# Optimization experiments

Measured on AMD Instinct MI355X. Metric: run time of the kernel, lower is better.

Reference implementation:

```python
import jax, jax.numpy as jnp
import numpy as np

NUM_LAYERS = 4
HID = 512
EMB = 512
VOCAB = 50000
SOU_LEN = 256
TAR_LEN = 50
BATCH = 8
VEXT = VOCAB + SOU_LEN


def _gru_layer(x, h0, wih, whh, bih, bhh):
    # x: [B,T,in], h0: [B,H]; PyTorch GRU gate order: r, z, n
    def step(h, xt):
        gi = xt @ wih.T + bih
        gh = h @ whh.T + bhh
        ir, iz, inn = jnp.split(gi, 3, axis=-1)
        hr, hz, hn = jnp.split(gh, 3, axis=-1)
        r = jax.nn.sigmoid(ir + hr)
        z = jax.nn.sigmoid(iz + hz)
        n = jnp.tanh(inn + r * hn)
        h_new = (1.0 - z) * n + z * h
        return h_new, h_new
    _, ys = jax.lax.scan(step, h0, jnp.swapaxes(x, 0, 1))
    return jnp.swapaxes(ys, 0, 1)


def _forward(sou, tar, hidden, encoder_outputs, extended_length,
             emb, gru_wih, gru_whh, gru_bih, gru_bhh,
             fc_enc_w, fc_enc_b, fc_dec_w, fc_dec_b, v_w,
             fc_out1_w, fc_out1_b, fc_out2_w, fc_out2_b,
             g1_w, g1_b, g2_w, g2_b, g3_w, g3_b):
    emb = emb.at[0].set(0.0)  # padding_idx=0 (also zeroes its grad)
    tar_emb = emb[tar]  # [B,T,E]
    # pack_padded_sequence: only first `length` steps processed, rest padded with 0
    lengths = jnp.maximum(jnp.sum(tar > 0, axis=-1), 1)
    x = tar_emb
    for l in range(gru_wih.shape[0]):
        x = _gru_layer(x, hidden[l], gru_wih[l], gru_whh[l], gru_bih[l], gru_bhh[l])
    t_idx = jnp.arange(x.shape[1])
    dec_out = jnp.where((t_idx[None, :] < lengths[:, None])[:, :, None], x, 0.0)  # [B,T,H]
    # additive (Bahdanau) attention
    e1 = encoder_outputs @ fc_enc_w.T + fc_enc_b          # [B,S,H]
    e2 = dec_out @ fc_dec_w.T + fc_dec_b                  # [B,T,H]
    energy = jnp.tanh(e1[:, None, :, :] + e2[:, :, None, :])  # [B,T,S,H]
    scores = jnp.einsum('btsh,h->bts', energy, v_w)
    scores = jnp.where((sou == 0)[:, None, :], -jnp.inf, scores)
    atten = jax.nn.softmax(scores, axis=-1)               # [B,T,S]
    weighted = jnp.einsum('bts,bsh->bth', atten, encoder_outputs)
    all_out = jnp.concatenate([weighted, dec_out], axis=-1)  # [B,T,2H]
    mid = all_out @ fc_out2_w.T + fc_out2_b
    logits = mid @ fc_out1_w.T + fc_out1_b                # [B,T,VEXT]
    # extended-vocab mask (vectorized version of the per-batch python loop)
    col = jnp.arange(logits.shape[-1])
    valid = col[None, None, :] < (VOCAB + extended_length)[:, None, None]
    logits = jnp.where(valid, logits, -1e9)
    output_gen = jax.nn.softmax(logits, axis=-1)
    # copy mechanism: scatter-add attention into extended vocab (replaces sparse one-hot bmm)
    def _scatter(att_b, sou_b):
        return jnp.zeros((att_b.shape[0], VEXT), att_b.dtype).at[:, sou_b].add(att_b)
    output_copy = jax.vmap(_scatter)(atten, sou)          # [B,T,VEXT]
    gate = jax.nn.sigmoid(
        jnp.einsum('bth,h->bt', weighted, g1_w) + g1_b[0]
        + jnp.einsum('bth,h->bt', dec_out, g2_w) + g2_b[0]
        + jnp.einsum('bte,e->bt', tar_emb, g3_w) + g3_b[0])[:, :, None]
    output = (1.0 - gate) * output_gen + gate * output_copy
    return output, atten


def setup_inputs() -> dict:
    key = jax.random.key(0)
    ks = jax.random.split(key, 24)
    s = 0.02
    return {
        'sou': jax.random.randint(ks[0], (BATCH, SOU_LEN), 0, VEXT),
        'tar': jax.random.randint(ks[1], (BATCH, TAR_LEN), 0, VEXT),
        'hidden': jax.random.normal(ks[2], (NUM_LAYERS, BATCH, HID), jnp.float32),
        'encoder_outputs': jax.random.normal(ks[3], (BATCH, SOU_LEN, HID), jnp.float32),
        'extended_length': jax.random.randint(ks[4], (BATCH,), 0, SOU_LEN),
        'emb': jax.random.normal(ks[5], (VEXT, EMB), jnp.float32) * s,
        'gru_wih': jax.random.normal(ks[6], (NUM_LAYERS, 3 * HID, EMB), jnp.float32) * s,
        'gru_whh': jax.random.normal(ks[7], (NUM_LAYERS, 3 * HID, HID), jnp.float32) * s,
        'gru_bih': jax.random.normal(ks[8], (NUM_LAYERS, 3 * HID), jnp.float32) * s,
        'gru_bhh': jax.random.normal(ks[9], (NUM_LAYERS, 3 * HID), jnp.float32) * s,
        'fc_enc_w': jax.random.normal(ks[10], (HID, HID), jnp.float32) * s,
        'fc_enc_b': jax.random.normal(ks[11], (HID,), jnp.float32) * s,
        'fc_dec_w': jax.random.normal(ks[12], (HID, HID), jnp.float32) * s,
        'fc_dec_b': jax.random.normal(ks[13], (HID,), jnp.float32) * s,
        'v_w': jax.random.normal(ks[14], (HID,), jnp.float32) * s,
        'fc_out1_w': jax.random.normal(ks[15], (VEXT, HID), jnp.float32) * s,
        'fc_out1_b': jax.random.normal(ks[16], (VEXT,), jnp.float32) * s,
        'fc_out2_w': jax.random.normal(ks[17], (HID, 2 * HID), jnp.float32) * s,
        'fc_out2_b': jax.random.normal(ks[18], (HID,), jnp.float32) * s,
        'g1_w': jax.random.normal(ks[19], (HID,), jnp.float32) * s,
        'g1_b': jnp.zeros((1,), jnp.float32),
        'g2_w': jax.random.normal(ks[20], (HID,), jnp.float32) * s,
        'g2_b': jnp.zeros((1,), jnp.float32),
        'g3_w': jax.random.normal(ks[21], (EMB,), jnp.float32) * s,
        'g3_b': jnp.zeros((1,), jnp.float32),
    }


def reference(sou, tar, hidden, encoder_outputs, extended_length,
              emb, gru_wih, gru_whh, gru_bih, gru_bhh,
              fc_enc_w, fc_enc_b, fc_dec_w, fc_dec_b, v_w,
              fc_out1_w, fc_out1_b, fc_out2_w, fc_out2_b,
              g1_w, g1_b, g2_w, g2_b, g3_w, g3_b):
    return _forward(sou, tar, hidden, encoder_outputs, extended_length,
                    emb, gru_wih, gru_whh, gru_bih, gru_bhh,
                    fc_enc_w, fc_enc_b, fc_dec_w, fc_dec_b, v_w,
                    fc_out1_w, fc_out1_b, fc_out2_w, fc_out2_b,
                    g1_w, g1_b, g2_w, g2_b, g3_w, g3_b)
```

## Files before the change

### kernel.cpp

```cpp
#include <hip/hip_runtime.h>

typedef unsigned short u16;
typedef unsigned int u32;
typedef unsigned long long u64;

using bf16x8 = __attribute__((ext_vector_type(8))) short;
using f32x4  = __attribute__((ext_vector_type(4))) float;

#define VOCAB 50000
#define VEXT  50256
#define OUT_AT_OFF 20102400L

__device__ __forceinline__ u16 f2b(float f) {
  u32 x = __float_as_uint(f);
  u32 r = (x + 0x7fffu + ((x >> 16) & 1u)) >> 16;
  return (u16)r;
}

__device__ __forceinline__ u32 sload32(const u32* p) {
  return __hip_atomic_load(p, __ATOMIC_RELAXED, __HIP_MEMORY_SCOPE_SYSTEM);
}
__device__ __forceinline__ u64 sload64(const u64* p) {
  return __hip_atomic_load(p, __ATOMIC_RELAXED, __HIP_MEMORY_SCOPE_SYSTEM);
}
__device__ __forceinline__ void sstore64(u64* p, u64 v) {
  __hip_atomic_store(p, v, __ATOMIC_RELAXED, __HIP_MEMORY_SCOPE_SYSTEM);
}
__device__ __forceinline__ bf16x8 sload8x(const u64* p) {
  union { u64 u[2]; bf16x8 v; } x;
  x.u[0] = sload64(p); x.u[1] = sload64(p + 1);
  return x.v;
}
__device__ __forceinline__ void wait_cnt(const u32* c, u32 target) {
  unsigned it = 0;
  while (sload32(c) < target) {
    __builtin_amdgcn_s_sleep(2);
    if (++it > (1u << 20)) break;
  }
  asm volatile("" ::: "memory");
}

__global__ void k_conv(const float* __restrict__ src, u16* __restrict__ dst,
                       long realN, long totalN) {
  long i = (long)blockIdx.x * 256 + threadIdx.x;
  if (i >= totalN) return;
  float v = (i < realN) ? src[i] : 0.f;
  dst[i] = f2b(v);
}

__global__ void k_h0b(const float* __restrict__ hidden, u16* __restrict__ h0B) {
  int i = blockIdx.x * 256 + threadIdx.x;
  int l = i >> 13, rem = i & 8191, rr = rem >> 9, k = rem & 511;
  float v = (rr < 8) ? hidden[((long)l * 8 + rr) * 512 + k] : 0.f;
  h0B[i] = f2b(v);
}

__global__ __launch_bounds__(256) void k_prep(const int* __restrict__ tar,
                                              const float* __restrict__ emb,
                                              const float* __restrict__ g3w,
                                              u16* __restrict__ xB0,
                                              float* __restrict__ g3dot) {
  int r = blockIdx.x;
  int tid = threadIdx.x;
  int idx = tar[r];
  __shared__ float red[256];
  float p = 0.f;
  for (int k = tid; k < 512; k += 256) {
    float v = (idx == 0) ? 0.f : emb[(long)idx * 512 + k];
    xB0[(long)r * 512 + k] = f2b(v);
    p += v * g3w[k];
  }
  red[tid] = p; __syncthreads();
  for (int o = 128; o > 0; o >>= 1) { if (tid < o) red[tid] += red[tid + o]; __syncthreads(); }
  if (tid == 0) g3dot[r] = red[0];
}

__global__ void k_lengths(const int* __restrict__ tar, int* __restrict__ lens) {
  int b = threadIdx.x;
  if (b < 8) {
    int c = 0;
    for (int t = 0; t < 50; t++) c += (tar[b * 50 + t] > 0) ? 1 : 0;
    lens[b] = (c > 0) ? c : 1;
  }
}

__global__ __launch_bounds__(256) void k_mask(float* __restrict__ x4f,
                                              const int* __restrict__ lens) {
  int r = blockIdx.x, b = r / 50, t = r % 50;
  if (t >= lens[b])
    for (int k = threadIdx.x; k < 512; k += 256) x4f[(long)r * 512 + k] = 0.f;
}

__global__ __launch_bounds__(128, 1) void k_gru(
    const u16* __restrict__ wihB, const u16* __restrict__ whhB,
    const float* __restrict__ bih, const float* __restrict__ bhh,
    const float* __restrict__ hidden, const u16* __restrict__ h0B,
    u16* __restrict__ xB,
    u32* __restrict__ hX,
    float* __restrict__ x4f,
    u32* __restrict__ cnt)
{
  const int wg = blockIdx.x;
  const int l = wg >> 5;
  const int c0 = (wg & 31) << 4;
  const int tid = threadIdx.x;
  const int wv = tid >> 6;
  const int lane = tid & 63;
  const int lrow = lane & 15;
  const int q = lane >> 4;

  __shared__ float giX[2][3][16][16];

  const u16* Wsrc = (wv == 0 ? wihB : whhB) + (long)l * 1536 * 512;

  const int col = c0 + lrow;
  const float bir = bih[l * 1536 + col],         bhr = bhh[l * 1536 + col];
  const float biz = bih[l * 1536 + 512 + col],   bhz = bhh[l * 1536 + 512 + col];
  const float bin_ = bih[l * 1536 + 1024 + col], bhn = bhh[l * 1536 + 1024 + col];

  const u16* xin = xB + (long)l * 16 * 50 * 512;

  float hreg[4];
  if (wv == 1) {
#pragma unroll
    for (int rg = 0; rg < 4; rg++) {
      int bb = q * 4 + rg;
      hreg[rg] = (bb < 8) ? hidden[((long)l * 8 + bb) * 512 + col] : 0.f;
    }
  }

  for (int t = 0; t < 50; t++) {
    bf16x8 af[16];
    if (wv == 0) {
      if (l > 0) {
        wait_cnt(cnt + (l - 1) * 16, 32u * (u32)(t + 1));
        const u64* A64 = (const u64*)((const u32*)xin + (long)lrow * 50 * 256 + (long)t * 256);
#pragma unroll
        for (int ks = 0; ks < 16; ks++) af[ks] = sload8x(A64 + ks * 8 + q * 2);
      } else {
        const u16* Asrc = xin + (long)lrow * 50 * 512 + (long)t * 512;
#pragma unroll
        for (int ks = 0; ks < 16; ks++) af[ks] = *(const bf16x8*)(Asrc + ks * 32 + q * 8);
      }
    } else {
      if (t > 0) {
        wait_cnt(cnt + l * 16, 32u * (u32)t);
        const u64* H64 = (const u64*)(hX + (((long)l * 2 + ((t - 1) & 1)) * 16 + lrow) * 256);
#pragma unroll
        for (int ks = 0; ks < 16; ks++) af[ks] = sload8x(H64 + ks * 8 + q * 2);
      } else {
        const u16* Asrc = h0B + ((long)l * 16 + lrow) * 512;
#pragma unroll
        for (int ks = 0; ks < 16; ks++) af[ks] = *(const bf16x8*)(Asrc + ks * 32 + q * 8);
      }
    }

    f32x4 a0 = {0.f, 0.f, 0.f, 0.f}, a1 = {0.f, 0.f, 0.f, 0.f}, a2 = {0.f, 0.f, 0.f, 0.f};
#pragma unroll
    for (int ks = 0; ks < 16; ks++) {
      bf16x8 b0 = *(const bf16x8*)(Wsrc + (long)(0 * 512 + c0 + lrow) * 512 + ks * 32 + q * 8);
      bf16x8 b1 = *(const bf16x8*)(Wsrc + (long)(1 * 512 + c0 + lrow) * 512 + ks * 32 + q * 8);
      bf16x8 b2 = *(const bf16x8*)(Wsrc + (long)(2 * 512 + c0 + lrow) * 512 + ks * 32 + q * 8);
      a0 = __builtin_amdgcn_mfma_f32_16x16x32_bf16(af[ks], b0, a0, 0, 0, 0);
      a1 = __builtin_amdgcn_mfma_f32_16x16x32_bf16(af[ks], b1, a1, 0, 0, 0);
      a2 = __builtin_amdgcn_mfma_f32_16x16x32_bf16(af[ks], b2, a2, 0, 0, 0);
    }

    if (wv == 0) {
#pragma unroll
      for (int rg = 0; rg < 4; rg++) {
        giX[t & 1][0][q * 4 + rg][lrow] = a0[rg];
        giX[t & 1][1][q * 4 + rg][lrow] = a1[rg];
        giX[t & 1][2][q * 4 + rg][lrow] = a2[rg];
      }
    }
    __syncthreads();

    if (wv == 1) {
#pragma unroll
      for (int rg = 0; rg < 4; rg++) {
        int bb = q * 4 + rg;
        float hnew = 0.f;
        u16 hb16 = 0;
        if (bb < 8) {
          float gir = giX[t & 1][0][bb][lrow] + bir;
          float giz = giX[t & 1][1][bb][lrow] + biz;
          float gin = giX[t & 1][2][bb][lrow] + bin_;
          float ghr = a0[rg] + bhr;
          float ghz = a1[rg] + bhz;
          float ghn = a2[rg] + bhn;
          float hprev = hreg[rg];
          float rr = 1.f / (1.f + expf(-(gir + ghr)));
          float zz = 1.f / (1.f + expf(-(giz + ghz)));
          float nn = tanhf(gin + rr * ghn);
          hnew = (1.f - zz) * nn + zz * hprev;
          hreg[rg] = hnew;
          hb16 = f2b(hnew);
        }
        u32 p32 = (u32)hb16 | ((u32)(u16)__shfl_xor((int)hb16, 1) << 16);
        u64 p64 = (u64)p32 | ((u64)(u32)__shfl_xor((int)p32, 2) << 32);
        if (bb < 8) {
          if ((lrow & 3) == 0) {
            long slot = ((long)l * 2 + (t & 1)) * 16 + bb;
            sstore64((u64*)hX + slot * 128 + (col >> 2), p64);
            if (l < 3)
              sstore64((u64*)xB + ((((long)(l + 1) * 16 + bb) * 50 + t) * 128) + (col >> 2), p64);
          }
          if (l == 3) x4f[((long)bb * 50 + t) * 512 + col] = hnew;
        }
      }
      asm volatile("s_waitcnt vmcnt(0)" ::: "memory");
      if (lane == 0)
        __hip_atomic_fetch_add(cnt + (long)l * 16, 1u,
                               __ATOMIC_RELAXED, __HIP_MEMORY_SCOPE_SYSTEM);
    }
  }
}

__global__ __launch_bounds__(256, 2) void k_gemm_bf16(
    const u16* __restrict__ A, const u16* __restrict__ Bm,
    const float* __restrict__ bias, float* __restrict__ C,
    int M, int N, int K, int ldc)
{
  __shared__ __align__(16) u16 As[4096];
  __shared__ __align__(16) u16 Bs[4096];
  const int tid = threadIdx.x;
  const int wv = tid >> 6, lane = tid & 63;
  const int wm = wv >> 1, wn = wv & 1;
  const int lrow = lane & 15, q = lane >> 4;
  const int m0 = blockIdx.y * 128, n0 = blockIdx.x * 128;

  f32x4 acc[4][4];
#pragma unroll
  for (int i = 0; i < 4; i++)
#pragma unroll
    for (int j = 0; j < 4; j++) acc[i][j] = {0.f, 0.f, 0.f, 0.f};

  for (int k0 = 0; k0 < K; k0 += 32) {
#pragma unroll
    for (int i = 0; i < 2; i++) {
      int c = i * 256 + tid;
      int row = c >> 2, ko = (c & 3) << 3;
      *(uint4*)(As + c * 8) = *(const uint4*)(A + (long)(m0 + row) * K + k0 + ko);
      *(uint4*)(Bs + c * 8) = *(const uint4*)(Bm + (long)(n0 + row) * K + k0 + ko);
    }
    __syncthreads();
    bf16x8 af[4], bfr[4];
#pragma unroll
    for (int i = 0; i < 4; i++) af[i] = *(const bf16x8*)(As + (wm * 64 + i * 16 + lrow) * 32 + q * 8);
#pragma unroll
    for (int j = 0; j < 4; j++) bfr[j] = *(const bf16x8*)(Bs + (wn * 64 + j * 16 + lrow) * 32 + q * 8);
#pragma unroll
    for (int i = 0; i < 4; i++)
#pragma unroll
      for (int j = 0; j < 4; j++)
        acc[i][j] = __builtin_amdgcn_mfma_f32_16x16x32_bf16(af[i], bfr[j], acc[i][j], 0, 0, 0);
    __syncthreads();
  }

#pragma unroll
  for (int i = 0; i < 4; i++) {
    int rbase = m0 + wm * 64 + i * 16 + q * 4;
#pragma unroll
    for (int j = 0; j < 4; j++) {
      int colg = n0 + wn * 64 + j * 16 + lrow;
      if (colg < N) {
        float bv = bias[colg];
#pragma unroll
        for (int rg = 0; rg < 4; rg++) {
          int rowg = rbase + rg;
          if (rowg < M) C[(long)rowg * ldc + colg] = acc[i][j][rg] + bv;
        }
      }
    }
  }
}

__global__ __launch_bounds__(256) void k_attn(
    const float* __restrict__ e1, const float* __restrict__ e2,
    const float* __restrict__ enc, const float* __restrict__ x4f,
    const int* __restrict__ sou, const float* __restrict__ vw,
    const float* __restrict__ g1w, const float* __restrict__ g1b,
    const float* __restrict__ g2w, const float* __restrict__ g2b,
    const float* __restrict__ g3b, const float* __restrict__ g3dot,
    float* __restrict__ all_out, float* __restrict__ gate,
    float* __restrict__ atten_out)
{
  int r = blockIdx.x;
  int b = r / 50;
  int tid = threadIdx.x;
  __shared__ float e2s[512], decs[512], at[256], red[256];
  for (int k = tid; k < 512; k += 256) {
    e2s[k] = e2[(long)r * 512 + k];
    decs[k] = x4f[(long)r * 512 + k];
  }
  __syncthreads();
  const float* erow = e1 + ((long)b * 256 + tid) * 512;
  float sc = 0.f;
#pragma unroll 4
  for (int h = 0; h < 512; h++) sc += vw[h] * tanhf(erow[h] + e2s[h]);
  if (sou[b * 256 + tid] == 0) sc = -INFINITY;

  red[tid] = sc; __syncthreads();
  for (int o = 128; o > 0; o >>= 1) { if (tid < o) red[tid] = fmaxf(red[tid], red[tid + o]); __syncthreads(); }
  float mx = red[0]; __syncthreads();
  float p = expf(sc - mx);
  red[tid] = p; __syncthreads();
  for (int o = 128; o > 0; o >>= 1) { if (tid < o) red[tid] += red[tid + o]; __syncthreads(); }
  float S = red[0]; __syncthreads();
  float a = p / S;
  at[tid] = a;
  atten_out[(long)r * 256 + tid] = a;
  __syncthreads();

  float pg = 0.f;
  for (int h = tid; h < 512; h += 256) {
    float wsum = 0.f;
    const float* ecol = enc + (long)b * 256 * 512 + h;
    for (int s = 0; s < 256; s++) wsum += at[s] * ecol[(long)s * 512];
    all_out[(long)r * 1024 + h] = wsum;
    all_out[(long)r * 1024 + 512 + h] = decs[h];
    pg += wsum * g1w[h] + decs[h] * g2w[h];
  }
  red[tid] = pg; __syncthreads();
  for (int o = 128; o > 0; o >>= 1) { if (tid < o) red[tid] += red[tid + o]; __syncthreads(); }
  if (tid == 0) {
    float z = red[0] + g1b[0] + g2b[0] + g3dot[r] + g3b[0];
    gate[r] = 1.f / (1.f + expf(-z));
  }
}

__global__ __launch_bounds__(1024) void k_softmax(float* __restrict__ out,
                                                  const float* __restrict__ gate,
                                                  const int* __restrict__ ext) {
  int r = blockIdx.x;
  int b = r / 50;
  int tid = threadIdx.x;
  int nv = VOCAB + ext[b];
  __shared__ float red[1024];
  float* row = out + (long)r * VEXT;
  float m = -INFINITY;
  for (int c = tid; c < nv; c += 1024) m = fmaxf(m, row[c]);
  red[tid] = m; __syncthreads();
  for (int o = 512; o > 0; o >>= 1) { if (tid < o) red[tid] = fmaxf(red[tid], red[tid + o]); __syncthreads(); }
  m = red[0]; __syncthreads();
  float s = 0.f;
  for (int c = tid; c < nv; c += 1024) s += expf(row[c] - m);
  red[tid] = s; __syncthreads();
  for (int o = 512; o > 0; o >>= 1) { if (tid < o) red[tid] += red[tid + o]; __syncthreads(); }
  float inv = (1.f - gate[r]) / red[0];
  for (int c = tid; c < VEXT; c += 1024) {
    float v = (c < nv) ? expf(row[c] - m) * inv : 0.f;
    row[c] = v;
  }
}

__global__ void k_scatter(float* __restrict__ out, const float* __restrict__ atten,
                          const float* __restrict__ gate, const int* __restrict__ sou) {
  int r = blockIdx.x, s = threadIdx.x;
  int b = r / 50;
  float v = gate[r] * atten[(long)r * 256 + s];
  int colv = sou[b * 256 + s];
  atomicAdd(out + (long)r * VEXT + colv, v);
}

extern "C" void kernel_launch(void* const* d_in, const int* in_sizes, int n_in,
                              void* d_out, int out_size, void* d_ws, size_t ws_size,
                              hipStream_t stream) {
  (void)in_sizes; (void)n_in; (void)out_size;
  const int* sou = (const int*)d_in[0];
  const int* tar = (const int*)d_in[1];
  const float* hidden = (const float*)d_in[2];
  const float* enc = (const float*)d_in[3];
  const int* ext = (const int*)d_in[4];
  const float* emb = (const float*)d_in[5];
  const float* wih = (const float*)d_in[6];
  const float* whh = (const float*)d_in[7];
  const float* bih = (const float*)d_in[8];
  const float* bhh = (const float*)d_in[9];
  const float* fc_enc_w = (const float*)d_in[10];
  const float* fc_enc_b = (const float*)d_in[11];
  const float* fc_dec_w = (const float*)d_in[12];
  const float* fc_dec_b = (const float*)d_in[13];
  const float* v_w = (const float*)d_in[14];
  const float* w1 = (const float*)d_in[15];
  const float* b1 = (const float*)d_in[16];
  const float* w2 = (const float*)d_in[17];
  const float* b2 = (const float*)d_in[18];
  const float* g1w = (const float*)d_in[19];
  const float* g1b = (const float*)d_in[20];
  const float* g2w = (const float*)d_in[21];
  const float* g2b = (const float*)d_in[22];
  const float* g3w = (const float*)d_in[23];
  const float* g3b = (const float*)d_in[24];
  float* out = (float*)d_out;

  char* base = (char*)d_ws;
  size_t cur = 0;
  auto alloc = [&](size_t bytes) -> void* {
    void* r = base + cur;
    cur = (cur + bytes + 255) & ~(size_t)255;
    return r;
  };
  u16* wihB = (u16*)alloc(6291456);
  u16* whhB = (u16*)alloc(6291456);
  u16* w1B  = (u16*)alloc(51511296);
  u16* encB = (u16*)alloc(2097152);
  u16* fceB = (u16*)alloc(524288);
  u16* fcdB = (u16*)alloc(524288);
  u16* fo2B = (u16*)alloc(1048576);
  u16* midB = (u16*)alloc(524288);
  u16* decB = (u16*)alloc(524288);
  u16* allB = (u16*)alloc(1048576);
  u16* xB   = (u16*)alloc(3276800);
  u16* h0B  = (u16*)alloc(65536);
  u32* hX   = (u32*)alloc(131072);
  float* x4f = (float*)alloc(819200);
  float* e1 = (float*)alloc(4194304);
  float* e2 = (float*)alloc(819200);
  float* allo = (float*)alloc(1638400);
  float* mid = (float*)alloc(819200);
  float* g3dot = (float*)alloc(1600);
  float* gate = (float*)alloc(1600);
  int* lens = (int*)alloc(32);
  u32* cnt = (u32*)alloc(256);
  if (cur > ws_size) return;

  hipMemsetAsync(cnt, 0, 256, stream);

  k_conv<<<12288, 256, 0, stream>>>(wih, wihB, 3145728L, 3145728L);
  k_conv<<<12288, 256, 0, stream>>>(whh, whhB, 3145728L, 3145728L);
  k_conv<<<100608, 256, 0, stream>>>(w1, w1B, 25731072L, 25755648L);
  k_conv<<<4096, 256, 0, stream>>>(enc, encB, 1048576L, 1048576L);
  k_conv<<<1024, 256, 0, stream>>>(fc_enc_w, fceB, 262144L, 262144L);
  k_conv<<<1024, 256, 0, stream>>>(fc_dec_w, fcdB, 262144L, 262144L);
  k_conv<<<2048, 256, 0, stream>>>(w2, fo2B, 524288L, 524288L);
  k_h0b<<<128, 256, 0, stream>>>(hidden, h0B);
  k_prep<<<400, 256, 0, stream>>>(tar, emb, g3w, xB, g3dot);
  k_lengths<<<1, 64, 0, stream>>>(tar, lens);

  k_gru<<<128, 128, 0, stream>>>(wihB, whhB, bih, bhh, hidden, h0B, xB, hX, x4f, cnt);
  k_mask<<<400, 256, 0, stream>>>(x4f, lens);
  k_conv<<<1024, 256, 0, stream>>>(x4f, decB, 204800L, 262144L);

  k_gemm_bf16<<<dim3(4, 16), 256, 0, stream>>>(encB, fceB, fc_enc_b, e1, 2048, 512, 512, 512);
  k_gemm_bf16<<<dim3(4, 4), 256, 0, stream>>>(decB, fcdB, fc_dec_b, e2, 400, 512, 512, 512);
  k_attn<<<400, 256, 0, stream>>>(e1, e2, enc, x4f, sou, v_w, g1w, g1b, g2w, g2b, g3b,
                                  g3dot, allo, gate, out + OUT_AT_OFF);
  k_conv<<<2048, 256, 0, stream>>>(allo, allB, 409600L, 524288L);
  k_gemm_bf16<<<dim3(4, 4), 256, 0, stream>>>(allB, fo2B, b2, mid, 400, 512, 1024, 512);
  k_conv<<<1024, 256, 0, stream>>>(mid, midB, 204800L, 262144L);

  k_gemm_bf16<<<dim3(393, 4), 256, 0, stream>>>(midB, w1B, b1, out, 400, 50256, 512, 50256);
  k_softmax<<<400, 1024, 0, stream>>>(out, gate, ext);
  k_scatter<<<400, 256, 0, stream>>>(out, out + OUT_AT_OFF, gate, sou);
}
```

Before: 1.107 ms.

## Replace GRU counter barriers with step-tagged data words polled directly

```diff
diff --git a/kernel.cpp b/kernel.cpp
--- a/kernel.cpp
+++ b/kernel.cpp
@@ -17,27 +17,11 @@
   return (u16)r;
 }
 
-__device__ __forceinline__ u32 sload32(const u32* p) {
-  return __hip_atomic_load(p, __ATOMIC_RELAXED, __HIP_MEMORY_SCOPE_SYSTEM);
-}
 __device__ __forceinline__ u64 sload64(const u64* p) {
   return __hip_atomic_load(p, __ATOMIC_RELAXED, __HIP_MEMORY_SCOPE_SYSTEM);
 }
 __device__ __forceinline__ void sstore64(u64* p, u64 v) {
   __hip_atomic_store(p, v, __ATOMIC_RELAXED, __HIP_MEMORY_SCOPE_SYSTEM);
-}
-__device__ __forceinline__ bf16x8 sload8x(const u64* p) {
-  union { u64 u[2]; bf16x8 v; } x;
-  x.u[0] = sload64(p); x.u[1] = sload64(p + 1);
-  return x.v;
-}
-__device__ __forceinline__ void wait_cnt(const u32* c, u32 target) {
-  unsigned it = 0;
-  while (sload32(c) < target) {
-    __builtin_amdgcn_s_sleep(2);
-    if (++it > (1u << 20)) break;
-  }
-  asm volatile("" ::: "memory");
 }
 
 __global__ void k_conv(const float* __restrict__ src, u16* __restrict__ dst,
@@ -95,10 +79,10 @@
     const u16* __restrict__ wihB, const u16* __restrict__ whhB,
     const float* __restrict__ bih, const float* __restrict__ bhh,
     const float* __restrict__ hidden, const u16* __restrict__ h0B,
-    u16* __restrict__ xB,
-    u32* __restrict__ hX,
-    float* __restrict__ x4f,
-    u32* __restrict__ cnt)
+    const u16* __restrict__ xB0,
+    u64* __restrict__ hXT,
+    u64* __restrict__ xT,
+    float* __restrict__ x4f)
 {
   const int wg = blockIdx.x;
   const int l = wg >> 5;
@@ -118,8 +102,6 @@
   const float biz = bih[l * 1536 + 512 + col],   bhz = bhh[l * 1536 + 512 + col];
   const float bin_ = bih[l * 1536 + 1024 + col], bhn = bhh[l * 1536 + 1024 + col];
 
-  const u16* xin = xB + (long)l * 16 * 50 * 512;
-
   float hreg[4];
   if (wv == 1) {
 #pragma unroll
@@ -131,27 +113,42 @@
 
   for (int t = 0; t < 50; t++) {
     bf16x8 af[16];
-    if (wv == 0) {
-      if (l > 0) {
-        wait_cnt(cnt + (l - 1) * 16, 32u * (u32)(t + 1));
-        const u64* A64 = (const u64*)((const u32*)xin + (long)lrow * 50 * 256 + (long)t * 256);
-#pragma unroll
-        for (int ks = 0; ks < 16; ks++) af[ks] = sload8x(A64 + ks * 8 + q * 2);
+    bool plain = (wv == 0) ? (l == 0) : (t == 0);
+    if (plain) {
+      const u16* Asrc = (wv == 0) ? (xB0 + (long)lrow * 50 * 512 + (long)t * 512)
+                                  : (h0B + ((long)l * 16 + lrow) * 512);
+#pragma unroll
+      for (int ks = 0; ks < 16; ks++) af[ks] = *(const bf16x8*)(Asrc + ks * 32 + q * 8);
+    } else {
+      const u64* S;
+      u32 want;
+      if (wv == 0) { S = xT + ((((long)(l - 1) * 8 + lrow) * 50) + t) * 256; want = (u32)(t + 1); }
+      else         { S = hXT + (((long)l * 2 + ((t - 1) & 1)) * 8 + lrow) * 256; want = (u32)t; }
+      union { u32 w[4]; bf16x8 v; } fr[16];
+      unsigned it = 0;
+      while (true) {
+        bool okl = true;
+        if (lrow < 8) {
+#pragma unroll
+          for (int ks = 0; ks < 16; ks++) {
+#pragma unroll
+            for (int j = 0; j < 4; j++) {
+              u64 tv = sload64(S + ks * 16 + q * 4 + j);
+              okl &= ((u32)(tv >> 32) == want);
+              fr[ks].w[j] = (u32)tv;
+            }
+          }
+        }
+        if (__all((int)okl)) break;
+        __builtin_amdgcn_s_sleep(1);
+        if (++it > (1u << 20)) break;
+      }
+      if (lrow < 8) {
+#pragma unroll
+        for (int ks = 0; ks < 16; ks++) af[ks] = fr[ks].v;
       } else {
-        const u16* Asrc = xin + (long)lrow * 50 * 512 + (long)t * 512;
-#pragma unroll
-        for (int ks = 0; ks < 16; ks++) af[ks] = *(const bf16x8*)(Asrc + ks * 32 + q * 8);
-      }
-    } else {
-      if (t > 0) {
-        wait_cnt(cnt + l * 16, 32u * (u32)t);
-        const u64* H64 = (const u64*)(hX + (((long)l * 2 + ((t - 1) & 1)) * 16 + lrow) * 256);
-#pragma unroll
-        for (int ks = 0; ks < 16; ks++) af[ks] = sload8x(H64 + ks * 8 + q * 2);
-      } else {
-        const u16* Asrc = h0B + ((long)l * 16 + lrow) * 512;
-#pragma unroll
-        for (int ks = 0; ks < 16; ks++) af[ks] = *(const bf16x8*)(Asrc + ks * 32 + q * 8);
+#pragma unroll
+        for (int ks = 0; ks < 16; ks++) af[ks] = bf16x8{0, 0, 0, 0, 0, 0, 0, 0};
       }
     }
 
@@ -198,21 +195,16 @@
           hb16 = f2b(hnew);
         }
         u32 p32 = (u32)hb16 | ((u32)(u16)__shfl_xor((int)hb16, 1) << 16);
-        u64 p64 = (u64)p32 | ((u64)(u32)__shfl_xor((int)p32, 2) << 32);
         if (bb < 8) {
-          if ((lrow & 3) == 0) {
-            long slot = ((long)l * 2 + (t & 1)) * 16 + bb;
-            sstore64((u64*)hX + slot * 128 + (col >> 2), p64);
+          if ((lane & 1) == 0) {
+            u64 tv = ((u64)(u32)(t + 1) << 32) | (u64)p32;
+            sstore64(hXT + (((long)l * 2 + (t & 1)) * 8 + bb) * 256 + ((c0 + lrow) >> 1), tv);
             if (l < 3)
-              sstore64((u64*)xB + ((((long)(l + 1) * 16 + bb) * 50 + t) * 128) + (col >> 2), p64);
+              sstore64(xT + ((((long)l * 8 + bb) * 50) + t) * 256 + ((c0 + lrow) >> 1), tv);
           }
           if (l == 3) x4f[((long)bb * 50 + t) * 512 + col] = hnew;
         }
       }
-      asm volatile("s_waitcnt vmcnt(0)" ::: "memory");
-      if (lane == 0)
-        __hip_atomic_fetch_add(cnt + (long)l * 16, 1u,
-                               __ATOMIC_RELAXED, __HIP_MEMORY_SCOPE_SYSTEM);
     }
   }
 }
@@ -412,9 +404,10 @@
   u16* midB = (u16*)alloc(524288);
   u16* decB = (u16*)alloc(524288);
   u16* allB = (u16*)alloc(1048576);
-  u16* xB   = (u16*)alloc(3276800);
+  u16* xB0  = (u16*)alloc(819200);
   u16* h0B  = (u16*)alloc(65536);
-  u32* hX   = (u32*)alloc(131072);
+  u64* hXT  = (u64*)alloc(131072);
+  u64* xT   = (u64*)alloc(2457600);
   float* x4f = (float*)alloc(819200);
   float* e1 = (float*)alloc(4194304);
   float* e2 = (float*)alloc(819200);
@@ -423,10 +416,9 @@
   float* g3dot = (float*)alloc(1600);
   float* gate = (float*)alloc(1600);
   int* lens = (int*)alloc(32);
-  u32* cnt = (u32*)alloc(256);
   if (cur > ws_size) return;
 
-  hipMemsetAsync(cnt, 0, 256, stream);
+  hipMemsetAsync(hXT, 0, 131072 + 2457600, stream);
 
   k_conv<<<12288, 256, 0, stream>>>(wih, wihB, 3145728L, 3145728L);
   k_conv<<<12288, 256, 0, stream>>>(whh, whhB, 3145728L, 3145728L);
@@ -436,10 +428,10 @@
   k_conv<<<1024, 256, 0, stream>>>(fc_dec_w, fcdB, 262144L, 262144L);
   k_conv<<<2048, 256, 0, stream>>>(w2, fo2B, 524288L, 524288L);
   k_h0b<<<128, 256, 0, stream>>>(hidden, h0B);
-  k_prep<<<400, 256, 0, stream>>>(tar, emb, g3w, xB, g3dot);
+  k_prep<<<400, 256, 0, stream>>>(tar, emb, g3w, xB0, g3dot);
   k_lengths<<<1, 64, 0, stream>>>(tar, lens);
 
-  k_gru<<<128, 128, 0, stream>>>(wihB, whhB, bih, bhh, hidden, h0B, xB, hX, x4f, cnt);
+  k_gru<<<128, 128, 0, stream>>>(wihB, whhB, bih, bhh, hidden, h0B, xB0, hXT, xT, x4f);
   k_mask<<<400, 256, 0, stream>>>(x4f, lens);
   k_conv<<<1024, 256, 0, stream>>>(x4f, decB, 204800L, 262144L);
 
```

After: 1.175 ms. 6.1% more time.
